# Kernel optimization log

Measured on AMD Instinct MI355X. Metric: run time of the kernel, lower is better.

## Reference

```python
import math
import jax, jax.numpy as jnp
import numpy as np

B, T, D, M, S = 2, 4096, 1024, 256, 8
BEAM = 4
TAU = 1.0


def setup_inputs() -> dict:
    key = jax.random.key(0)
    ks = jax.random.split(key, 24)
    std = 0.02
    inp = {
        "mu": jax.random.normal(ks[0], (B, T, D), jnp.float32),
        "lam": jax.random.uniform(ks[1], (B, T, D), jnp.float32),
        "pi": jax.random.uniform(ks[2], (B, T, 7), jnp.float32),
        "pi_write": jax.random.uniform(ks[3], (B, T, 1), jnp.float32),
        "Wq": jax.random.normal(ks[4], (M, D), jnp.float32) * std,
        "bq": jnp.zeros((M,), jnp.float32),
        "Wk": jax.random.normal(ks[5], (M, D), jnp.float32) * std,
        "bk": jnp.zeros((M,), jnp.float32),
        "Wv": jax.random.normal(ks[6], (M, D), jnp.float32) * std,
        "bv": jnp.zeros((M,), jnp.float32),
        "Wo": jax.random.normal(ks[7], (D, M), jnp.float32) * std,
        "bo": jnp.zeros((D,), jnp.float32),
        "Ws1": jax.random.normal(ks[8], (256, 2 * D + 7), jnp.float32) * std,
        "bs1": jnp.zeros((256,), jnp.float32),
        "Ws2": jax.random.normal(ks[9], (1, 256), jnp.float32) * std,
        "bs2": jnp.zeros((1,), jnp.float32),
        "Wsr": jax.random.normal(ks[10], (M, M), jnp.float32) * std,
        "bsr": jnp.zeros((M,), jnp.float32),
        "scratch_init": jax.random.normal(ks[11], (1, S, M), jnp.float32) * 0.02,
        "gate": jnp.float32(-5.0),
    }
    return inp


def _build_tree(k, v, w):
    """Causal binary tree of weighted span summaries. Level 0 = leaves."""
    levels = [(k, v, w)]
    while k.shape[1] > 1:
        n = k.shape[1]
        if n % 2 == 1:
            pad = ((0, 0), (0, 1), (0, 0))
            k = jnp.pad(k, pad); v = jnp.pad(v, pad); w = jnp.pad(w, pad)
        k1, k2 = k[:, 0::2], k[:, 1::2]
        v1, v2 = v[:, 0::2], v[:, 1::2]
        w1, w2 = w[:, 0::2], w[:, 1::2]
        tw = w1 + w2 + 1e-8
        k = (w1 * k1 + w2 * k2) / tw
        v = (w1 * v1 + w2 * v2) / tw
        w = tw
        levels.append((k, v, w))
    return levels


def _retrieve_at_level(q, keys, values, beam):
    Bq, Tq, Mq = q.shape
    n = keys.shape[1]
    scores = jnp.einsum('btm,bnm->btn', q, keys) / math.sqrt(Mq)
    if n <= Tq:  # causal: query i may only see slot j <= i
        mask = jnp.arange(n)[None, :] > jnp.arange(Tq)[:, None]
        scores = jnp.where(mask[None], -jnp.inf, scores)
    kk = min(beam, n)
    if n > kk:
        vals, idx = jax.lax.top_k(scores, kk)           # (B,T,k)
        p = jax.nn.softmax(vals, axis=-1)               # == softmax of scattered sparse scores
        v_sel = jnp.take_along_axis(values[:, None], idx[..., None], axis=2)  # (B,T,k,M)
        return jnp.einsum('btk,btkm->btm', p, v_sel)
    attn = jax.nn.softmax(scores, axis=-1)
    return jnp.einsum('btn,bnm->btm', attn, values)


def reference(mu, lam, pi, pi_write, Wq, bq, Wk, bk, Wv, bv, Wo, bo,
              Ws1, bs1, Ws2, bs2, Wsr, bsr, scratch_init, gate):
    # ---- write: build causal tree from detached keys/values ----
    mu_d = jax.lax.stop_gradient(mu)
    w0 = jax.lax.stop_gradient(pi_write)                # (B,T,1)
    k = mu_d @ Wk.T + bk
    v = mu_d @ Wv.T + bv
    tree = _build_tree(k, v, w0)

    # ---- read ----
    q = mu @ Wq.T + bq                                  # (B,T,M)
    log_var = -jnp.log(jnp.clip(lam, 1e-6))
    si = jnp.concatenate([mu, log_var, pi], axis=-1)    # (B,T,2D+7)
    h = si @ Ws1.T + bs1
    h = h * jax.nn.sigmoid(h)                           # SiLU
    s = jax.nn.sigmoid((h @ Ws2.T + bs2)[..., 0])       # (B,T)

    scratch = jnp.broadcast_to(scratch_init, (mu.shape[0], S, M))
    sq = q @ Wsr.T + bsr
    sattn = jax.nn.softmax(jnp.einsum('btm,bsm->bts', sq, scratch) / math.sqrt(M), axis=-1)
    scratch_ctx = jnp.einsum('bts,bsm->btm', sattn, scratch)

    level_ctx = [_retrieve_at_level(q, lk, lv, BEAM) for (lk, lv, _) in tree]
    level_stack = jnp.stack(level_ctx, axis=2)          # (B,T,L,M)
    L = level_stack.shape[2]
    level_idx = jnp.arange(L, dtype=mu.dtype)
    s_scaled = s[..., None] * (L - 1)                   # (B,T,1)
    kappa = jnp.exp(-0.5 * ((level_idx - s_scaled) / TAU) ** 2)
    kappa = kappa / jnp.clip(kappa.sum(axis=-1, keepdims=True), 1e-8)
    tree_ctx = jnp.einsum('btl,btlm->btm', kappa, level_stack)

    blend = s[..., None]
    combined = (1.0 - blend) * tree_ctx + blend * scratch_ctx
    out = combined @ Wo.T + bo
    return jax.nn.sigmoid(gate) * out                   # (B,T,D)
```

## Files before the change

### kernel.cpp

```cpp
#include <hip/hip_runtime.h>
#include <math.h>

#define TT 4096
#define BB 2
#define MMDIM 256
#define RTOT 8192
#define NSLICE 39

typedef __attribute__((ext_vector_type(8))) short short8_t;
typedef __attribute__((ext_vector_type(4))) float f32x4;

__device__ __forceinline__ unsigned short f2bf(float x)
{
    unsigned u = __float_as_uint(x);
    u += 0x7fffu + ((u >> 16) & 1u);
    return (unsigned short)(u >> 16);
}

__global__ __launch_bounds__(256) void gemm_qk(
    const float* __restrict__ mu, const float* __restrict__ Wq,
    const float* __restrict__ bq, const float* __restrict__ Wk,
    const float* __restrict__ bk, float* __restrict__ q_, float* __restrict__ k_,
    unsigned short* __restrict__ qkh, unsigned short* __restrict__ qkl)
{
    __shared__ float As[2][8][68];
    __shared__ float Ws[2][8][132];
    const int tid = threadIdx.x;
    const int tx = tid & 15;
    const int ty = tid >> 4;
    const int r0 = blockIdx.x * 64;
    const int c0 = blockIdx.y * 128;
    const bool isq = (c0 < 256);

    const float* W = isq ? (Wq + (size_t)c0 * 1024)
                         : (Wk + (size_t)(c0 - 256) * 1024);
    const float* bias = isq ? (bq + c0) : (bk + (c0 - 256));

    const bool isA = (tid < 128);
    const int sArow = tid >> 1, sAk = (tid & 1) * 4;
    const int sWrow = tid >> 1, sWk = (tid & 1) * 4;

    float acc[4][8] = {};
    float4 rA, rW;

    if (isA) rA = *(const float4*)&mu[(size_t)(r0 + sArow) * 1024 + sAk];
    rW = *(const float4*)&W[(size_t)sWrow * 1024 + sWk];
    if (isA) {
        As[0][sAk + 0][sArow] = rA.x; As[0][sAk + 1][sArow] = rA.y;
        As[0][sAk + 2][sArow] = rA.z; As[0][sAk + 3][sArow] = rA.w;
    }
    Ws[0][sWk + 0][sWrow] = rW.x; Ws[0][sWk + 1][sWrow] = rW.y;
    Ws[0][sWk + 2][sWrow] = rW.z; Ws[0][sWk + 3][sWrow] = rW.w;
    __syncthreads();

    int buf = 0;
    for (int k0 = 0; k0 < 1024; k0 += 8) {
        const bool has = (k0 + 8 < 1024);
        if (has) {
            if (isA) rA = *(const float4*)&mu[(size_t)(r0 + sArow) * 1024 + k0 + 8 + sAk];
            rW = *(const float4*)&W[(size_t)sWrow * 1024 + k0 + 8 + sWk];
        }
        #pragma unroll
        for (int kk = 0; kk < 8; ++kk) {
            float4 a  = *(const float4*)&As[buf][kk][ty * 4];
            float4 b0 = *(const float4*)&Ws[buf][kk][tx * 8];
            float4 b1 = *(const float4*)&Ws[buf][kk][tx * 8 + 4];
            float av[4] = {a.x, a.y, a.z, a.w};
            float bv[8] = {b0.x, b0.y, b0.z, b0.w, b1.x, b1.y, b1.z, b1.w};
            #pragma unroll
            for (int i = 0; i < 4; ++i)
                #pragma unroll
                for (int j = 0; j < 8; ++j)
                    acc[i][j] += av[i] * bv[j];
        }
        if (has) {
            int nb = buf ^ 1;
            if (isA) {
                As[nb][sAk + 0][sArow] = rA.x; As[nb][sAk + 1][sArow] = rA.y;
                As[nb][sAk + 2][sArow] = rA.z; As[nb][sAk + 3][sArow] = rA.w;
            }
            Ws[nb][sWk + 0][sWrow] = rW.x; Ws[nb][sWk + 1][sWrow] = rW.y;
            Ws[nb][sWk + 2][sWrow] = rW.z; Ws[nb][sWk + 3][sWrow] = rW.w;
        }
        __syncthreads();
        buf ^= 1;
    }

    const int lcol = (c0 & 255) + tx * 8;
    #pragma unroll
    for (int i = 0; i < 4; ++i) {
        int row = r0 + ty * 4 + i;
        float o[8];
        #pragma unroll
        for (int j = 0; j < 8; ++j) o[j] = acc[i][j] + bias[tx * 8 + j];
        float* dst = isq ? &q_[(size_t)row * MMDIM + lcol]
                         : &k_[(size_t)row * MMDIM + lcol];
        *(float4*)dst       = make_float4(o[0], o[1], o[2], o[3]);
        *(float4*)(dst + 4) = make_float4(o[4], o[5], o[6], o[7]);
        size_t srow = isq ? (size_t)row : (size_t)(RTOT + row);
        short8_t sh, sl;
        #pragma unroll
        for (int j = 0; j < 8; ++j) {
            unsigned short h = f2bf(o[j]);
            sh[j] = (short)h;
            sl[j] = (short)f2bf(o[j] - __uint_as_float((unsigned)h << 16));
        }
        *(short8_t*)&qkh[srow * MMDIM + lcol] = sh;
        *(short8_t*)&qkl[srow * MMDIM + lcol] = sl;
    }
}

__global__ __launch_bounds__(256) void convert_split(
    const float* __restrict__ src, unsigned short* __restrict__ hi,
    unsigned short* __restrict__ lo, int n4)
{
    int i = blockIdx.x * 256 + threadIdx.x;
    if (i >= n4) return;
    float4 x = ((const float4*)src)[i];
    ushort4 h, l;
    h.x = f2bf(x.x); l.x = f2bf(x.x - __uint_as_float((unsigned)h.x << 16));
    h.y = f2bf(x.y); l.y = f2bf(x.y - __uint_as_float((unsigned)h.y << 16));
    h.z = f2bf(x.z); l.z = f2bf(x.z - __uint_as_float((unsigned)h.z << 16));
    h.w = f2bf(x.w); l.w = f2bf(x.w - __uint_as_float((unsigned)h.w << 16));
    ((ushort4*)hi)[i] = h;
    ((ushort4*)lo)[i] = l;
}

__global__ __launch_bounds__(256) void pad_ws1_split(
    const float* __restrict__ src, unsigned short* __restrict__ hi,
    unsigned short* __restrict__ lo)
{
    const int r = blockIdx.x;
    for (int c = threadIdx.x; c < 2112; c += 256) {
        float v = (c < 2055) ? src[(size_t)r * 2055 + c] : 0.f;
        unsigned short h = f2bf(v);
        hi[(size_t)r * 2112 + c] = h;
        lo[(size_t)r * 2112 + c] = f2bf(v - __uint_as_float((unsigned)h << 16));
    }
}

template<int ASRC, int WITH_GATE>
__global__ __launch_bounds__(256) void gemm_mfma(
    const float* __restrict__ A, const float* __restrict__ lam,
    const float* __restrict__ pi,
    const unsigned short* __restrict__ Wh, const unsigned short* __restrict__ Wl,
    const float* __restrict__ bias, const float* __restrict__ gate,
    float* __restrict__ C, int K, int N)
{
    __shared__ unsigned short Ah[64][72], Al[64][72];
    __shared__ unsigned short Bh[128][72], Bl[128][72];
    const int tid = threadIdx.x;
    const int lane = tid & 63;
    const int wv = tid >> 6;
    const int r0 = blockIdx.x * 64;
    const int c0 = blockIdx.y * 128;

    f32x4 acc0[8] = {}, acc1[8] = {}, acc2[8] = {};

    const int arow = wv * 16 + (lane & 15);
    const int koff = (lane >> 4) * 8;

    for (int kc = 0; kc < K; kc += 64) {
        #pragma unroll
        for (int i = 0; i < 2; ++i) {
            int g = tid + i * 256;
            int row = g >> 3, gq = g & 7;
            float x[8];
            if (ASRC == 0) {
                float4 v0 = *(const float4*)&A[(size_t)(r0 + row) * K + kc + gq * 8];
                float4 v1 = *(const float4*)&A[(size_t)(r0 + row) * K + kc + gq * 8 + 4];
                x[0] = v0.x; x[1] = v0.y; x[2] = v0.z; x[3] = v0.w;
                x[4] = v1.x; x[5] = v1.y; x[6] = v1.z; x[7] = v1.w;
            } else {
                #pragma unroll
                for (int e = 0; e < 8; ++e) {
                    int c = kc + gq * 8 + e;
                    float val;
                    if (c < 1024)      val = A[(size_t)(r0 + row) * 1024 + c];
                    else if (c < 2048) val = -logf(fmaxf(lam[(size_t)(r0 + row) * 1024 + (c - 1024)], 1e-6f));
                    else if (c < 2055) val = pi[(size_t)(r0 + row) * 7 + (c - 2048)];
                    else               val = 0.f;
                    x[e] = val;
                }
            }
            short8_t sh, sl;
            #pragma unroll
            for (int e = 0; e < 8; ++e) {
                unsigned short h = f2bf(x[e]);
                sh[e] = (short)h;
                sl[e] = (short)f2bf(x[e] - __uint_as_float((unsigned)h << 16));
            }
            *(short8_t*)&Ah[row][gq * 8] = sh;
            *(short8_t*)&Al[row][gq * 8] = sl;
        }
        #pragma unroll
        for (int i = 0; i < 4; ++i) {
            int g = tid + i * 256;
            int row = g >> 3, gq = g & 7;
            *(short8_t*)&Bh[row][gq * 8] = *(const short8_t*)&Wh[(size_t)(c0 + row) * K + kc + gq * 8];
            *(short8_t*)&Bl[row][gq * 8] = *(const short8_t*)&Wl[(size_t)(c0 + row) * K + kc + gq * 8];
        }
        __syncthreads();
        #pragma unroll
        for (int kt = 0; kt < 2; ++kt) {
            short8_t afh = *(const short8_t*)&Ah[arow][kt * 32 + koff];
            short8_t afl = *(const short8_t*)&Al[arow][kt * 32 + koff];
            #pragma unroll
            for (int ct = 0; ct < 8; ++ct) {
                short8_t bh = *(const short8_t*)&Bh[ct * 16 + (lane & 15)][kt * 32 + koff];
                short8_t bl = *(const short8_t*)&Bl[ct * 16 + (lane & 15)][kt * 32 + koff];
                acc0[ct] = __builtin_amdgcn_mfma_f32_16x16x32_bf16(afh, bh, acc0[ct], 0, 0, 0);
                acc1[ct] = __builtin_amdgcn_mfma_f32_16x16x32_bf16(afl, bh, acc1[ct], 0, 0, 0);
                acc2[ct] = __builtin_amdgcn_mfma_f32_16x16x32_bf16(afh, bl, acc2[ct], 0, 0, 0);
            }
        }
        __syncthreads();
    }

    float g = 1.f;
    if (WITH_GATE) g = 1.f / (1.f + expf(-gate[0]));
    #pragma unroll
    for (int ct = 0; ct < 8; ++ct) {
        int col = c0 + ct * 16 + (lane & 15);
        float b = bias[col];
        #pragma unroll
        for (int r = 0; r < 4; ++r) {
            int row = r0 + wv * 16 + (lane >> 4) * 4 + r;
            C[(size_t)row * N + col] = (acc0[ct][r] + acc1[ct][r] + acc2[ct][r] + b) * g;
        }
    }
}

__global__ __launch_bounds__(256) void s_kernel(
    const float* __restrict__ h, const float* __restrict__ Ws2,
    const float* __restrict__ bs2, float* __restrict__ sb,
    float* __restrict__ kap)
{
    const int tid = threadIdx.x;
    const int wave = tid >> 6, lane = tid & 63;
    const int t = blockIdx.x * 4 + wave;

    float4 hv = *(const float4*)&h[(size_t)t * MMDIM + lane * 4];
    float4 wv = *(const float4*)&Ws2[lane * 4];
    float p = 0.f;
    p += (hv.x / (1.f + expf(-hv.x))) * wv.x;
    p += (hv.y / (1.f + expf(-hv.y))) * wv.y;
    p += (hv.z / (1.f + expf(-hv.z))) * wv.z;
    p += (hv.w / (1.f + expf(-hv.w))) * wv.w;
    #pragma unroll
    for (int o = 32; o; o >>= 1) p += __shfl_xor(p, o);

    float z = p + bs2[0];
    float s = 1.f / (1.f + expf(-z));
    float c = s * 12.f;
    float Z = 0.f;
    #pragma unroll
    for (int l = 0; l < 13; ++l) {
        float d = (float)l - c;
        Z += expf(-0.5f * d * d);
    }
    Z = fmaxf(Z, 1e-8f);
    if (lane < 13) {
        float d = (float)lane - c;
        kap[(size_t)t * 16 + lane] = (1.f - s) * expf(-0.5f * d * d) / Z;
    }
    if (lane == 0) sb[t] = s;
}

__global__ __launch_bounds__(256) void scratch_kernel(
    const float* __restrict__ sq, const float* __restrict__ scr,
    const float* __restrict__ sb, float* __restrict__ ctx)
{
    const int tid = threadIdx.x;
    const int wave = tid >> 6, lane = tid & 63;
    const int t = blockIdx.x * 4 + wave;

    float4 qv = *(const float4*)&sq[(size_t)t * MMDIM + lane * 4];
    float4 fr[8];
    float sc[8];
    #pragma unroll
    for (int s = 0; s < 8; ++s) {
        fr[s] = *(const float4*)&scr[s * MMDIM + lane * 4];
        sc[s] = qv.x * fr[s].x + qv.y * fr[s].y + qv.z * fr[s].z + qv.w * fr[s].w;
    }
    #pragma unroll
    for (int s = 0; s < 8; ++s) {
        #pragma unroll
        for (int o = 32; o; o >>= 1) sc[s] += __shfl_xor(sc[s], o);
        sc[s] *= 0.0625f;
    }
    float mx = sc[0];
    #pragma unroll
    for (int s = 1; s < 8; ++s) mx = fmaxf(mx, sc[s]);
    float sum = 0.f;
    #pragma unroll
    for (int s = 0; s < 8; ++s) { sc[s] = expf(sc[s] - mx); sum += sc[s]; }
    float inv = 1.f / sum;
    float blend = sb[t];
    float4 o = {0, 0, 0, 0};
    #pragma unroll
    for (int s = 0; s < 8; ++s) {
        float pp = sc[s] * inv;
        o.x += pp * fr[s].x; o.y += pp * fr[s].y;
        o.z += pp * fr[s].z; o.w += pp * fr[s].w;
    }
    o.x *= blend; o.y *= blend; o.z *= blend; o.w *= blend;
    *(float4*)&ctx[(size_t)t * MMDIM + lane * 4] = o;
}

__global__ __launch_bounds__(256) void wtree_kernel(
    const float* __restrict__ pw, float* __restrict__ wtree)
{
    __shared__ float wa[4096];
    __shared__ float wb2[2048];
    const int b = blockIdx.x;
    const int tid = threadIdx.x;
    for (int t = tid; t < 4096; t += 256) wa[t] = pw[b * 4096 + t];
    __syncthreads();
    int n = 4096, lvl = 1;
    float* cur = wa; float* nxt = wb2;
    while (n > 1) {
        int nout = n >> 1;
        int off = TT - (8192 >> lvl);
        for (int j = tid; j < nout; j += 256) {
            float t = cur[2 * j] + cur[2 * j + 1] + 1e-8f;
            nxt[j] = t;
            wtree[b * 4095 + off + j] = t;
        }
        __syncthreads();
        float* tmp = cur; cur = nxt; nxt = tmp;
        n = nout; ++lvl;
    }
}

__global__ __launch_bounds__(256) void tree_level(
    const float* __restrict__ kin, const float* __restrict__ vin,
    const float* __restrict__ win, float* __restrict__ kout,
    float* __restrict__ vout, int in_bs, int win_bs, int out_bs)
{
    const int j = blockIdx.x;
    const int b = blockIdx.y;
    const int tid = threadIdx.x;
    const float* wp = win + (size_t)b * win_bs;
    float w1 = wp[2 * j], w2 = wp[2 * j + 1];
    float tw = w1 + w2 + 1e-8f;
    size_t i1 = ((size_t)b * in_bs + 2 * j) * MMDIM + tid;
    size_t io = ((size_t)b * out_bs + j) * MMDIM + tid;
    kout[io] = (w1 * kin[i1] + w2 * kin[i1 + MMDIM]) / tw;
    vout[io] = (w1 * vin[i1] + w2 * vin[i1 + MMDIM]) / tw;
}

__global__ __launch_bounds__(256) void tree_mid(
    float* __restrict__ kt_, float* __restrict__ vt_,
    const float* __restrict__ wtree)
{
    __shared__ float kb[128][68];
    __shared__ float vb[128][68];
    const int tid = threadIdx.x;
    const int g  = blockIdx.x >> 2;
    const int mc = blockIdx.x & 3;
    const int b  = blockIdx.y;
    const int wb = b * 4095;

    for (int idx = tid; idx < 64 * 64; idx += 256) {
        int j = idx >> 6, m = idx & 63;
        size_t gi = (size_t)(wb + g * 64 + j) * MMDIM + mc * 64 + m;
        kb[j][m] = kt_[gi];
        vb[j][m] = vt_[gi];
    }
    __syncthreads();

    int pb = 0;
    for (int l = 2; l <= 6; ++l) {
        int nloc = 64 >> (l - 1);
        int cb = 128 - (128 >> (l - 1));
        int offm1 = TT - (8192 >> (l - 1));
        int offl  = TT - (8192 >> l);
        int gbase = g * nloc;
        for (int idx = tid; idx < nloc * 64; idx += 256) {
            int j = idx >> 6, m = idx & 63;
            float w1 = wtree[wb + offm1 + (gbase + j) * 2];
            float w2 = wtree[wb + offm1 + (gbase + j) * 2 + 1];
            float tw = wtree[wb + offl + gbase + j];
            float kvv = (w1 * kb[pb + 2 * j][m] + w2 * kb[pb + 2 * j + 1][m]) / tw;
            float vvv = (w1 * vb[pb + 2 * j][m] + w2 * vb[pb + 2 * j + 1][m]) / tw;
            kb[cb + j][m] = kvv;
            vb[cb + j][m] = vvv;
            size_t go = (size_t)(wb + offl + gbase + j) * MMDIM + mc * 64 + m;
            kt_[go] = kvv;
            vt_[go] = vvv;
        }
        __syncthreads();
        pb = cb;
    }
}

__global__ __launch_bounds__(256) void tree_deep(
    float* __restrict__ kt_, float* __restrict__ vt_,
    const float* __restrict__ wtree)
{
    __shared__ float kb[128][68];
    __shared__ float vb[128][68];
    const int tid = threadIdx.x;
    const int mc = blockIdx.x;
    const int b = blockIdx.y;
    const int wb = b * 4095;

    for (int idx = tid; idx < 64 * 64; idx += 256) {
        int j = idx >> 6, m = idx & 63;
        size_t gi = (size_t)(wb + 3968 + j) * MMDIM + mc * 64 + m;
        kb[j][m] = kt_[gi];
        vb[j][m] = vt_[gi];
    }
    __syncthreads();

    int pb = 0;
    for (int l = 7; l <= 12; ++l) {
        int nout = 4096 >> l;
        int cb = 128 - (128 >> (l - 6));
        int offm1 = TT - (8192 >> (l - 1));
        int offl  = TT - (8192 >> l);
        for (int idx = tid; idx < nout * 64; idx += 256) {
            int j = idx >> 6, m = idx & 63;
            float w1 = wtree[wb + offm1 + 2 * j];
            float w2 = wtree[wb + offm1 + 2 * j + 1];
            float tw = wtree[wb + offl + j];
            float kvv = (w1 * kb[pb + 2 * j][m] + w2 * kb[pb + 2 * j + 1][m]) / tw;
            float vvv = (w1 * vb[pb + 2 * j][m] + w2 * vb[pb + 2 * j + 1][m]) / tw;
            kb[cb + j][m] = kvv;
            vb[cb + j][m] = vvv;
            size_t go = (size_t)(wb + offl + j) * MMDIM + mc * 64 + m;
            kt_[go] = kvv;
            vt_[go] = vvv;
        }
        __syncthreads();
        pb = cb;
    }
}

__device__ __forceinline__ unsigned long long pack_key(float v, int col)
{
    unsigned u = __float_as_uint(v);
    u ^= ((unsigned)((int)u >> 31)) | 0x80000000u;
    return ((unsigned long long)u << 32) | (unsigned)(~col);
}

__device__ __forceinline__ void unpack_key(unsigned long long k, float& v, int& col)
{
    unsigned u = (unsigned)(k >> 32);
    u ^= (u & 0x80000000u) ? 0x80000000u : 0xFFFFFFFFu;
    v = __uint_as_float(u);
    col = (int)(~(unsigned)k);
}

__device__ __forceinline__ unsigned long long shfl_xor_u64(unsigned long long v, int off)
{
    int lo = __shfl_xor((int)(unsigned)v, off);
    int hi = __shfl_xor((int)(v >> 32), off);
    return ((unsigned long long)(unsigned)hi << 32) | (unsigned)lo;
}

__device__ __forceinline__ void ins4u(unsigned long long k, unsigned long long t[4])
{
    if (k <= t[3]) return;
    t[3] = k;
    if (t[3] > t[2]) { unsigned long long x = t[2]; t[2] = t[3]; t[3] = x; }
    if (t[2] > t[1]) { unsigned long long x = t[1]; t[1] = t[2]; t[2] = x; }
    if (t[1] > t[0]) { unsigned long long x = t[0]; t[0] = t[1]; t[1] = x; }
}

__device__ __forceinline__ void ins5u(unsigned long long k, unsigned long long t[5])
{
    if (k <= t[4]) return;
    t[4] = k;
    if (t[4] > t[3]) { unsigned long long x = t[3]; t[3] = t[4]; t[4] = x; }
    if (t[3] > t[2]) { unsigned long long x = t[2]; t[2] = t[3]; t[3] = x; }
    if (t[2] > t[1]) { unsigned long long x = t[1]; t[1] = t[2]; t[2] = x; }
    if (t[1] > t[0]) { unsigned long long x = t[0]; t[0] = t[1]; t[1] = x; }
}

__device__ __forceinline__ bool beats(float v, int id, float v2, int id2)
{
    return (v > v2) || (v == v2 && id < id2);
}

__device__ __forceinline__ void ins5(float v, int id, float tv[5], int ti[5])
{
    if (!beats(v, id, tv[4], ti[4])) return;
    tv[4] = v; ti[4] = id;
    #pragma unroll
    for (int s = 4; s > 0; --s) {
        if (beats(tv[s], ti[s], tv[s - 1], ti[s - 1])) {
            float fv = tv[s]; tv[s] = tv[s - 1]; tv[s - 1] = fv;
            int iv = ti[s]; ti[s] = ti[s - 1]; ti[s - 1] = iv;
        }
    }
}

__device__ __forceinline__ void slice_map(int sid, int& level, int& c0)
{
    if (sid < 16)      { level = 0; c0 = sid << 8; }
    else if (sid < 24) { level = 1; c0 = (sid - 16) << 8; }
    else if (sid < 28) { level = 2; c0 = (sid - 24) << 8; }
    else if (sid < 30) { level = 3; c0 = (sid - 28) << 8; }
    else               { level = sid - 26; c0 = 0; }
}

__global__ __launch_bounds__(512) void topk_mfma(
    const unsigned short* __restrict__ qkh, const unsigned short* __restrict__ qkl,
    const unsigned short* __restrict__ kth, const unsigned short* __restrict__ ktl,
    float2* __restrict__ topw)
{
    __shared__ unsigned short kbh[2][32][256];
    __shared__ unsigned short kbl[2][32][256];

    const int tid = threadIdx.x;
    const int lane = tid & 63;
    const int wv = tid >> 6;
    const int r0 = blockIdx.x * 128;
    const int sid = blockIdx.y;
    const int b = r0 >> 12;
    const int t0 = r0 & 4095;

    int level, c0b;
    slice_map(sid, level, c0b);
    const int n = TT >> level;
    const int nv = min(min(n, t0 + 128), c0b + 256);

    if (c0b >= nv) {
        if (tid < 128) {
            float2 e = make_float2(-INFINITY, __int_as_float(0x7fffffff));
            #pragma unroll
            for (int s = 0; s < 5; ++s)
                topw[(size_t)(sid * 5 + s) * RTOT + r0 + tid] = e;
        }
        return;
    }

    const unsigned short* Kh;
    const unsigned short* Kl;
    if (level == 0) {
        Kh = qkh + (size_t)RTOT * MMDIM + (size_t)b * TT * MMDIM;
        Kl = qkl + (size_t)RTOT * MMDIM + (size_t)b * TT * MMDIM;
    } else {
        size_t off = (size_t)b * 4095 + (TT - (8192 >> level));
        Kh = kth + off * MMDIM;
        Kl = ktl + off * MMDIM;
    }

    const int arow = r0 + wv * 16 + (lane & 15);
    const int koff = (lane >> 4) * 8;
    short8_t ah[8], al[8];
    #pragma unroll
    for (int kt = 0; kt < 8; ++kt) {
        ah[kt] = *(const short8_t*)(qkh + (size_t)arow * MMDIM + kt * 32 + koff);
        al[kt] = *(const short8_t*)(qkl + (size_t)arow * MMDIM + kt * 32 + koff);
    }

    unsigned long long tk[4][4] = {};
    const int trow0 = t0 + wv * 16 + (lane >> 4) * 4;

    auto stage = [&](int c0, int bf) {
        #pragma unroll
        for (int j = 0; j < 2; ++j) {
            int base = (wv * 2 + j) * 1024;
            int bidx = base + lane * 16;
            int r = bidx >> 9;
            int x = bidx & 511;
            int csrc = x ^ ((r & 7) << 4);
            int cc = min(c0 + r, n - 1);
            const char* gh = (const char*)(Kh + (size_t)cc * MMDIM) + csrc;
            const char* gl = (const char*)(Kl + (size_t)cc * MMDIM) + csrc;
            char* lh = (char*)&kbh[bf][0][0] + base;
            char* ll = (char*)&kbl[bf][0][0] + base;
            __builtin_amdgcn_global_load_lds(
                (const __attribute__((address_space(1))) unsigned int*)gh,
                (__attribute__((address_space(3))) unsigned int*)lh, 16, 0, 0);
            __builtin_amdgcn_global_load_lds(
                (const __attribute__((address_space(1))) unsigned int*)gl,
                (__attribute__((address_space(3))) unsigned int*)ll, 16, 0, 0);
        }
    };

    stage(c0b, 0);
    __syncthreads();

    int buf = 0;
    for (int c0 = c0b; c0 < nv; c0 += 32) {
        const bool has = (c0 + 32 < nv);
        if (has) stage(c0 + 32, buf ^ 1);

        #pragma unroll
        for (int ct = 0; ct < 2; ++ct) {
            f32x4 a0 = {0.f, 0.f, 0.f, 0.f};
            f32x4 a1 = {0.f, 0.f, 0.f, 0.f};
            f32x4 a2 = {0.f, 0.f, 0.f, 0.f};
            const int bc = ct * 16 + (lane & 15);
            const int swz = (bc & 7) << 3;
            #pragma unroll
            for (int kt = 0; kt < 8; ++kt) {
                int sidx = (kt * 32 + koff) ^ swz;
                short8_t bh = *(const short8_t*)&kbh[buf][bc][sidx];
                short8_t bl = *(const short8_t*)&kbl[buf][bc][sidx];
                a0 = __builtin_amdgcn_mfma_f32_16x16x32_bf16(ah[kt], bh, a0, 0, 0, 0);
                a1 = __builtin_amdgcn_mfma_f32_16x16x32_bf16(al[kt], bh, a1, 0, 0, 0);
                a2 = __builtin_amdgcn_mfma_f32_16x16x32_bf16(ah[kt], bl, a2, 0, 0, 0);
            }
            const int col = c0 + bc;
            #pragma unroll
            for (int r = 0; r < 4; ++r) {
                float sc = (a0[r] + a1[r] + a2[r]) * 0.0625f;
                unsigned long long key =
                    (col <= trow0 + r && col < n) ? pack_key(sc, col) : 0ull;
                if (__any(key > tk[r][3])) ins4u(key, tk[r]);
            }
        }
        __syncthreads();
        buf ^= 1;
    }

    #pragma unroll
    for (int r = 0; r < 4; ++r) {
        unsigned long long k5[5];
        #pragma unroll
        for (int s = 0; s < 4; ++s) k5[s] = tk[r][s];
        k5[4] = 0ull;
        #pragma unroll
        for (int pass = 0; pass < 4; ++pass) {
            int off = 1 << pass;
            unsigned long long o[5];
            #pragma unroll
            for (int s = 0; s < 5; ++s) o[s] = shfl_xor_u64(k5[s], off);
            #pragma unroll
            for (int s = 0; s < 5; ++s) ins5u(o[s], k5);
        }
        if ((lane & 15) == 0) {
            int row = r0 + wv * 16 + (lane >> 4) * 4 + r;
            #pragma unroll
            for (int s = 0; s < 5; ++s) {
                float2 e;
                if (k5[s] == 0ull) {
                    e = make_float2(-INFINITY, __int_as_float(0x7fffffff));
                } else {
                    float v; int c;
                    unpack_key(k5[s], v, c);
                    e = make_float2(v, __int_as_float(c));
                }
                topw[(size_t)(sid * 5 + s) * RTOT + row] = e;
            }
        }
    }
}

__global__ __launch_bounds__(256) void merge_gather(
    const float2* __restrict__ topw, const float* __restrict__ q,
    const float* __restrict__ kl0, const float* __restrict__ ktf,
    const float* __restrict__ vl0, const float* __restrict__ vtree,
    const float* __restrict__ kap, float* __restrict__ ctx)
{
    const int tid = threadIdx.x;
    const int lane = tid & 63;
    const int wv = __builtin_amdgcn_readfirstlane(tid >> 6);
    const int row = blockIdx.x * 4 + wv;
    const int b = row >> 12;

    float cr[4] = {0, 0, 0, 0};
    const float4 q4 = *(const float4*)&q[(size_t)row * MMDIM + lane * 4];

    for (int l = 0; l <= 12; ++l) {
        int s0, cnt;
        if (l == 0)      { s0 = 0;  cnt = 16; }
        else if (l == 1) { s0 = 16; cnt = 8; }
        else if (l == 2) { s0 = 24; cnt = 4; }
        else if (l == 3) { s0 = 28; cnt = 2; }
        else             { s0 = 26 + l; cnt = 1; }

        float tv[5]; int ti[5];
        #pragma unroll
        for (int s = 0; s < 5; ++s) { tv[s] = -INFINITY; ti[s] = 0x7fffffff; }
        for (int sl = 0; sl < cnt; ++sl) {
            #pragma unroll
            for (int s = 0; s < 5; ++s) {
                float2 e = topw[(size_t)((s0 + sl) * 5 + s) * RTOT + row];
                if (e.x > -INFINITY) ins5(e.x, __float_as_int(e.y), tv, ti);
            }
        }

        const float* Kf = (l == 0)
            ? kl0 + (size_t)b * TT * MMDIM
            : ktf + ((size_t)b * 4095 + (TT - (8192 >> l))) * MMDIM;

        bool ambig = (l <= 9) && (tv[3] - tv[4] < 1e-4f);
        if (ambig) {
            float rv[5]; int ri[5];
            #pragma unroll
            for (int s = 0; s < 5; ++s) { rv[s] = -INFINITY; ri[s] = 0x7fffffff; }
            for (int sl = 0; sl < cnt; ++sl) {
                #pragma unroll
                for (int s = 0; s < 5; ++s) {
                    float2 e = topw[(size_t)((s0 + sl) * 5 + s) * RTOT + row];
                    if (e.x > -INFINITY) {
                        int idx = __float_as_int(e.y);
                        float4 k4 = *(const float4*)&Kf[(size_t)idx * MMDIM + lane * 4];
                        float p = q4.x * k4.x + q4.y * k4.y + q4.z * k4.z + q4.w * k4.w;
                        #pragma unroll
                        for (int o = 32; o; o >>= 1) p += __shfl_xor(p, o);
                        ins5(p * 0.0625f, idx, rv, ri);
                    }
                }
            }
            #pragma unroll
            for (int s = 0; s < 5; ++s) { tv[s] = rv[s]; ti[s] = ri[s]; }
        }

        float m0 = tv[0];
        float e0 = expf(tv[0] - m0);
        float e1 = expf(tv[1] - m0);
        float e2 = expf(tv[2] - m0);
        float e3 = expf(tv[3] - m0);
        float sum = e0 + e1 + e2 + e3;
        float kp = kap[(size_t)row * 16 + l];
        float scl = kp / sum;
        float ps[4] = {e0 * scl, e1 * scl, e2 * scl, e3 * scl};

        const float* Vb = (l == 0)
            ? vl0 + (size_t)b * TT * MMDIM
            : vtree + ((size_t)b * 4095 + (TT - (8192 >> l))) * MMDIM;

        #pragma unroll
        for (int s = 0; s < 4; ++s) {
            if (ps[s] > 0.f) {
                float4 vv = *(const float4*)&Vb[(size_t)ti[s] * MMDIM + lane * 4];
                cr[0] += ps[s] * vv.x; cr[1] += ps[s] * vv.y;
                cr[2] += ps[s] * vv.z; cr[3] += ps[s] * vv.w;
            }
        }
    }

    float* cp = ctx + (size_t)row * MMDIM + lane * 4;
    float4 c = *(float4*)cp;
    c.x += cr[0]; c.y += cr[1]; c.z += cr[2]; c.w += cr[3];
    *(float4*)cp = c;
}

extern "C" void kernel_launch(void* const* d_in, const int* in_sizes, int n_in,
                              void* d_out, int out_size, void* d_ws, size_t ws_size,
                              hipStream_t stream)
{
    const float* mu  = (const float*)d_in[0];
    const float* lam = (const float*)d_in[1];
    const float* pi  = (const float*)d_in[2];
    const float* pw  = (const float*)d_in[3];
    const float* Wq  = (const float*)d_in[4];
    const float* bq  = (const float*)d_in[5];
    const float* Wk  = (const float*)d_in[6];
    const float* bk  = (const float*)d_in[7];
    const float* Wv  = (const float*)d_in[8];
    const float* bv  = (const float*)d_in[9];
    const float* Wo  = (const float*)d_in[10];
    const float* bo  = (const float*)d_in[11];
    const float* Ws1 = (const float*)d_in[12];
    const float* bs1 = (const float*)d_in[13];
    const float* Ws2 = (const float*)d_in[14];
    const float* bs2 = (const float*)d_in[15];
    const float* Wsr = (const float*)d_in[16];
    const float* bsr = (const float*)d_in[17];
    const float* scr = (const float*)d_in[18];
    const float* gate = (const float*)d_in[19];
    float* out = (float*)d_out;

    float* w = (float*)d_ws;
    const size_t RM = (size_t)RTOT * MMDIM;
    float* q_   = w;  w += RM;
    float* k_   = w;  w += RM;
    float* v_   = w;  w += RM;
    float* h_   = w;  w += RM;
    float* sq_  = w;  w += RM;
    float* ctx_ = w;  w += RM;
    float* sb_  = w;  w += RTOT;
    float* kap_ = w;  w += (size_t)RTOT * 16;
    float* kt_  = w;  w += (size_t)BB * 4095 * MMDIM;
    float* vt_  = w;  w += (size_t)BB * 4095 * MMDIM;
    float* wtree_ = w; w += (size_t)BB * 4095;
    unsigned short* qkh_ = (unsigned short*)w;  w += RM;
    unsigned short* qkl_ = (unsigned short*)w;  w += RM;
    unsigned short* kth_ = (unsigned short*)w;  w += (size_t)BB * 4095 * MMDIM / 2;
    unsigned short* ktl_ = (unsigned short*)w;  w += (size_t)BB * 4095 * MMDIM / 2;
    float2* topw = (float2*)w;  w += (size_t)NSLICE * 5 * RTOT * 2;
    unsigned short* w1h_ = (unsigned short*)w;  w += (size_t)256 * 2112 / 2;
    unsigned short* w1l_ = (unsigned short*)w;  w += (size_t)256 * 2112 / 2;
    unsigned short* wvh_ = (unsigned short*)w;  w += (size_t)256 * 1024 / 2;
    unsigned short* wvl_ = (unsigned short*)w;  w += (size_t)256 * 1024 / 2;
    unsigned short* wsrh_ = (unsigned short*)w; w += (size_t)256 * 256 / 2;
    unsigned short* wsrl_ = (unsigned short*)w; w += (size_t)256 * 256 / 2;
    unsigned short* woh_ = (unsigned short*)w;  w += (size_t)1024 * 256 / 2;
    unsigned short* wol_ = (unsigned short*)w;  w += (size_t)1024 * 256 / 2;

    pad_ws1_split<<<256, 256, 0, stream>>>(Ws1, w1h_, w1l_);
    convert_split<<<256, 256, 0, stream>>>(Wv, wvh_, wvl_, 65536);
    convert_split<<<64, 256, 0, stream>>>(Wsr, wsrh_, wsrl_, 16384);
    convert_split<<<256, 256, 0, stream>>>(Wo, woh_, wol_, 65536);

    gemm_qk<<<dim3(128, 4), 256, 0, stream>>>(mu, Wq, bq, Wk, bk,
                                              q_, k_, qkh_, qkl_);
    gemm_mfma<0, 0><<<dim3(128, 2), 256, 0, stream>>>(mu, nullptr, nullptr, wvh_, wvl_,
                                                      bv, nullptr, v_, 1024, 256);
    gemm_mfma<1, 0><<<dim3(128, 2), 256, 0, stream>>>(mu, lam, pi, w1h_, w1l_,
                                                      bs1, nullptr, h_, 2112, 256);
    s_kernel<<<2048, 256, 0, stream>>>(h_, Ws2, bs2, sb_, kap_);
    gemm_mfma<0, 0><<<dim3(128, 2), 256, 0, stream>>>(q_, nullptr, nullptr, wsrh_, wsrl_,
                                                      bsr, nullptr, sq_, 256, 256);
    scratch_kernel<<<2048, 256, 0, stream>>>(sq_, scr, sb_, ctx_);

    wtree_kernel<<<BB, 256, 0, stream>>>(pw, wtree_);
    tree_level<<<dim3(2048, BB), 256, 0, stream>>>(k_, v_, pw, kt_, vt_,
                                                   TT, TT, 4095);
    tree_mid<<<dim3(128, BB), 256, 0, stream>>>(kt_, vt_, wtree_);
    tree_deep<<<dim3(4, BB), 256, 0, stream>>>(kt_, vt_, wtree_);

    convert_split<<<(int)(((size_t)BB * 4095 * MMDIM / 4 + 255) / 256), 256, 0, stream>>>(
        kt_, kth_, ktl_, (int)((size_t)BB * 4095 * MMDIM / 4));

    topk_mfma<<<dim3(64, NSLICE), 512, 0, stream>>>(qkh_, qkl_, kth_, ktl_, topw);
    merge_gather<<<2048, 256, 0, stream>>>(topw, q_, k_, kt_, v_, vt_, kap_, ctx_);
    gemm_mfma<0, 1><<<dim3(128, 8), 256, 0, stream>>>(ctx_, nullptr, nullptr, woh_, wol_,
                                                      bo, gate, out, 256, 1024);
}
```

Measured before the change: 856.3 us.

## Make topk per-wave independent tasks reading keys directly from global memory

Restructures the top-k scoring kernel so each wave owns a 16-row query tile for one slice, instead of eight waves sharing a 128-row tile. The causal trim now happens at a 16-row granularity, so less masked work is done. The LDS double-buffered staging and block barriers are removed, and each wave loads its key fragments straight from global memory into registers. Blocks are remapped with an XCD-style interleave across 4992 blocks of 256 threads. The cost is that key tiles are no longer shared across waves through LDS, so global and L2 traffic goes up and there is no explicit prefetch overlap.

```diff
diff --git a/kernel.cpp b/kernel.cpp
--- a/kernel.cpp
+++ b/kernel.cpp
@@ -506,33 +506,35 @@
     else               { level = sid - 26; c0 = 0; }
 }
 
-__global__ __launch_bounds__(512) void topk_mfma(
+__global__ __launch_bounds__(256) void topk_mfma(
     const unsigned short* __restrict__ qkh, const unsigned short* __restrict__ qkl,
     const unsigned short* __restrict__ kth, const unsigned short* __restrict__ ktl,
     float2* __restrict__ topw)
 {
-    __shared__ unsigned short kbh[2][32][256];
-    __shared__ unsigned short kbl[2][32][256];
-
     const int tid = threadIdx.x;
     const int lane = tid & 63;
     const int wv = tid >> 6;
-    const int r0 = blockIdx.x * 128;
-    const int sid = blockIdx.y;
+
+    const int hw = blockIdx.x;
+    const int logical = (hw & 7) * 624 + (hw >> 3);
+    const int task = logical * 4 + wv;
+    const int sid = task >> 9;
+    const int rg  = task & 511;
+    const int r0 = rg * 16;
     const int b = r0 >> 12;
     const int t0 = r0 & 4095;
 
     int level, c0b;
     slice_map(sid, level, c0b);
     const int n = TT >> level;
-    const int nv = min(min(n, t0 + 128), c0b + 256);
+    const int nv = min(min(n, t0 + 16), c0b + 256);
 
     if (c0b >= nv) {
-        if (tid < 128) {
+        if (lane < 16) {
             float2 e = make_float2(-INFINITY, __int_as_float(0x7fffffff));
             #pragma unroll
             for (int s = 0; s < 5; ++s)
-                topw[(size_t)(sid * 5 + s) * RTOT + r0 + tid] = e;
+                topw[(size_t)(sid * 5 + s) * RTOT + r0 + lane] = e;
         }
         return;
     }
@@ -548,7 +550,7 @@
         Kl = ktl + off * MMDIM;
     }
 
-    const int arow = r0 + wv * 16 + (lane & 15);
+    const int arow = r0 + (lane & 15);
     const int koff = (lane >> 4) * 8;
     short8_t ah[8], al[8];
     #pragma unroll
@@ -558,65 +560,37 @@
     }
 
     unsigned long long tk[4][4] = {};
-    const int trow0 = t0 + wv * 16 + (lane >> 4) * 4;
-
-    auto stage = [&](int c0, int bf) {
-        #pragma unroll
-        for (int j = 0; j < 2; ++j) {
-            int base = (wv * 2 + j) * 1024;
-            int bidx = base + lane * 16;
-            int r = bidx >> 9;
-            int x = bidx & 511;
-            int csrc = x ^ ((r & 7) << 4);
-            int cc = min(c0 + r, n - 1);
-            const char* gh = (const char*)(Kh + (size_t)cc * MMDIM) + csrc;
-            const char* gl = (const char*)(Kl + (size_t)cc * MMDIM) + csrc;
-            char* lh = (char*)&kbh[bf][0][0] + base;
-            char* ll = (char*)&kbl[bf][0][0] + base;
-            __builtin_amdgcn_global_load_lds(
-                (const __attribute__((address_space(1))) unsigned int*)gh,
-                (__attribute__((address_space(3))) unsigned int*)lh, 16, 0, 0);
-            __builtin_amdgcn_global_load_lds(
-                (const __attribute__((address_space(1))) unsigned int*)gl,
-                (__attribute__((address_space(3))) unsigned int*)ll, 16, 0, 0);
-        }
-    };
-
-    stage(c0b, 0);
-    __syncthreads();
-
-    int buf = 0;
-    for (int c0 = c0b; c0 < nv; c0 += 32) {
-        const bool has = (c0 + 32 < nv);
-        if (has) stage(c0 + 32, buf ^ 1);
-
-        #pragma unroll
-        for (int ct = 0; ct < 2; ++ct) {
-            f32x4 a0 = {0.f, 0.f, 0.f, 0.f};
-            f32x4 a1 = {0.f, 0.f, 0.f, 0.f};
-            f32x4 a2 = {0.f, 0.f, 0.f, 0.f};
-            const int bc = ct * 16 + (lane & 15);
-            const int swz = (bc & 7) << 3;
-            #pragma unroll
-            for (int kt = 0; kt < 8; ++kt) {
-                int sidx = (kt * 32 + koff) ^ swz;
-                short8_t bh = *(const short8_t*)&kbh[buf][bc][sidx];
-                short8_t bl = *(const short8_t*)&kbl[buf][bc][sidx];
-                a0 = __builtin_amdgcn_mfma_f32_16x16x32_bf16(ah[kt], bh, a0, 0, 0, 0);
-                a1 = __builtin_amdgcn_mfma_f32_16x16x32_bf16(al[kt], bh, a1, 0, 0, 0);
-                a2 = __builtin_amdgcn_mfma_f32_16x16x32_bf16(ah[kt], bl, a2, 0, 0, 0);
-            }
-            const int col = c0 + bc;
-            #pragma unroll
-            for (int r = 0; r < 4; ++r) {
-                float sc = (a0[r] + a1[r] + a2[r]) * 0.0625f;
-                unsigned long long key =
-                    (col <= trow0 + r && col < n) ? pack_key(sc, col) : 0ull;
-                if (__any(key > tk[r][3])) ins4u(key, tk[r]);
-            }
-        }
-        __syncthreads();
-        buf ^= 1;
+    const int trow0 = t0 + (lane >> 4) * 4;
+
+    for (int c0 = c0b; c0 < nv; c0 += 16) {
+        const int bc = min(c0 + (lane & 15), n - 1);
+        const unsigned short* gh = Kh + (size_t)bc * MMDIM + koff;
+        const unsigned short* gl = Kl + (size_t)bc * MMDIM + koff;
+        short8_t bh[8], bl[8];
+        #pragma unroll
+        for (int kt = 0; kt < 8; ++kt) {
+            bh[kt] = *(const short8_t*)(gh + kt * 32);
+            bl[kt] = *(const short8_t*)(gl + kt * 32);
+        }
+
+        f32x4 a0 = {0.f, 0.f, 0.f, 0.f};
+        f32x4 a1 = {0.f, 0.f, 0.f, 0.f};
+        f32x4 a2 = {0.f, 0.f, 0.f, 0.f};
+        #pragma unroll
+        for (int kt = 0; kt < 8; ++kt) {
+            a0 = __builtin_amdgcn_mfma_f32_16x16x32_bf16(ah[kt], bh[kt], a0, 0, 0, 0);
+            a1 = __builtin_amdgcn_mfma_f32_16x16x32_bf16(al[kt], bh[kt], a1, 0, 0, 0);
+            a2 = __builtin_amdgcn_mfma_f32_16x16x32_bf16(ah[kt], bl[kt], a2, 0, 0, 0);
+        }
+
+        const int col = c0 + (lane & 15);
+        #pragma unroll
+        for (int r = 0; r < 4; ++r) {
+            float sc = (a0[r] + a1[r] + a2[r]) * 0.0625f;
+            unsigned long long key =
+                (col <= trow0 + r && col < n) ? pack_key(sc, col) : 0ull;
+            if (__any(key > tk[r][3])) ins4u(key, tk[r]);
+        }
     }
 
     #pragma unroll
@@ -635,7 +609,7 @@
             for (int s = 0; s < 5; ++s) ins5u(o[s], k5);
         }
         if ((lane & 15) == 0) {
-            int row = r0 + wv * 16 + (lane >> 4) * 4 + r;
+            int row = r0 + (lane >> 4) * 4 + r;
             #pragma unroll
             for (int s = 0; s < 5; ++s) {
                 float2 e;
@@ -821,7 +795,7 @@
     convert_split<<<(int)(((size_t)BB * 4095 * MMDIM / 4 + 255) / 256), 256, 0, stream>>>(
         kt_, kth_, ktl_, (int)((size_t)BB * 4095 * MMDIM / 4));
 
-    topk_mfma<<<dim3(64, NSLICE), 512, 0, stream>>>(qkh_, qkl_, kth_, ktl_, topw);
+    topk_mfma<<<4992, 256, 0, stream>>>(qkh_, qkl_, kth_, ktl_, topw);
     merge_gather<<<2048, 256, 0, stream>>>(topw, q_, k_, kt_, v_, vt_, kap_, ctx_);
     gemm_mfma<0, 1><<<dim3(128, 8), 256, 0, stream>>>(ctx_, nullptr, nullptr, woh_, wol_,
                                                       bo, gate, out, 256, 1024);
```

Result: slower. 1.123 ms (+31.1%).
